# Kernel tuning notes

Measured on AMD Instinct MI355X. Metric: run time of the kernel, lower is better.

The kernel has to match this reference:

```python
import jax, jax.numpy as jnp
import numpy as np

NBIN = 256
EPS = 1e-10


def _diffhist(img, hmin, hmax):
    # Soft (linear-interpolation) histogram, faithful to torch index_add version.
    img = img.ravel()
    keep = (img >= hmin) & (img <= hmax)
    dh = (hmax - hmin) / (NBIN - 1)
    x = (img - hmin) / dh
    idx = jnp.floor(x)
    d = x - idx  # fractional part, carries the gradient
    # zero-weight + clamped index instead of boolean compaction (jit-friendly)
    idx_i = jnp.where(keep, idx.astype(jnp.int32), 0)
    w0 = jnp.where(keep, 1.0 - d, 0.0)
    w1 = jnp.where(keep, d, 0.0)
    h = jnp.zeros(NBIN + 1, dtype=img.dtype)
    h = h.at[idx_i].add(w0).at[idx_i + 1].add(w1)
    return h[:NBIN]


def setup_inputs() -> dict:
    key = jax.random.key(0)
    k0, k1 = jax.random.split(key)
    shape = (4, 256, 256, 256)
    img0 = jax.random.normal(k0, shape, dtype=jnp.float32)
    img1 = jax.random.normal(k1, shape, dtype=jnp.float32)
    return {"img0": img0, "img1": img1}


def reference(img0, img1):
    min0 = jnp.min(img0)  # differentiable, like torch.min
    h0 = _diffhist(img0, min0, 0.0)
    h1 = _diffhist(img1, min0, 0.0)
    h0 = (h0 + EPS) / (h0.sum() + EPS)
    h1 = (h1 + EPS) / (h1.sum() + EPS)
    # KLDivLoss(log_target=True, reduction='mean'):
    #   mean( exp(target) * (target - input) )
    inp = jnp.log((h1 + EPS) / h1)
    tgt = jnp.log((h1 + EPS) / h0)
    return jnp.mean(jnp.exp(tgt) * (tgt - inp))
```

## Files before the change

kernel.cpp:

```cpp
#include <hip/hip_runtime.h>

#define NBIN 256
#define EPSF 1e-10f
#define DSCALE 4096.0f
#define DSCALE_INV (1.0 / 4096.0)
#define DMASK ((1ull << 40) - 1)

__device__ __forceinline__ unsigned enc_f32(float f) {
    unsigned u = __float_as_uint(f);
    return (u & 0x80000000u) ? ~u : (u ^ 0x80000000u);
}
__device__ __forceinline__ float dec_f32(unsigned e) {
    unsigned u = (e & 0x80000000u) ? (e ^ 0x80000000u) : ~e;
    return __uint_as_float(u);
}

__global__ void init_kernel(unsigned* ws_min, unsigned long long* gh) {
    if (threadIdx.x == 0) *ws_min = 0xFFFFFFFFu;
    for (int j = threadIdx.x; j < 2 * NBIN; j += blockDim.x) gh[j] = 0ull;
}

__global__ void __launch_bounds__(256) min_kernel(const float4* __restrict__ img0,
                                                  long n4, unsigned* ws_min) {
    long stride = (long)gridDim.x * blockDim.x;
    long i = (long)blockIdx.x * blockDim.x + threadIdx.x;
    float m = __int_as_float(0x7f800000);
    if (i < n4) {
        float4 cur = img0[i];
        long j = i + stride;
        for (; j < n4; j += stride) {
            float4 nxt = img0[j];
            m = fminf(m, fminf(fminf(cur.x, cur.y), fminf(cur.z, cur.w)));
            cur = nxt;
        }
        m = fminf(m, fminf(fminf(cur.x, cur.y), fminf(cur.z, cur.w)));
    }
    for (int off = 32; off; off >>= 1) m = fminf(m, __shfl_xor(m, off));
    __shared__ float sm[4];
    int lane = threadIdx.x & 63, wid = threadIdx.x >> 6;
    if (lane == 0) sm[wid] = m;
    __syncthreads();
    if (threadIdx.x == 0) {
        float bm = fminf(fminf(sm[0], sm[1]), fminf(sm[2], sm[3]));
        atomicMin(ws_min, enc_f32(bm));
    }
}

__device__ __forceinline__ void hadd(float v, float hmin, float inv_dh,
                                     unsigned* h) {
    if (v >= hmin && v <= 0.f) {
        float x = (v - hmin) * inv_dh;
        float fi = floorf(x);
        int idx = (int)fi;
        unsigned di = __float2uint_rn((x - fi) * DSCALE);
        atomicAdd(&h[idx], (1u << 24) | di);
    }
}

__global__ void __launch_bounds__(256) hist_kernel(const float4* __restrict__ img0,
                                                   const float4* __restrict__ img1,
                                                   long n4, const unsigned* ws_min,
                                                   unsigned long long* __restrict__ gh) {
    __shared__ unsigned lh[4][2][NBIN];
    int tid = threadIdx.x;
    int wid = tid >> 6;
    unsigned* base = &lh[0][0][0];
    for (int j = tid; j < 4 * 2 * NBIN; j += 256) base[j] = 0u;
    __syncthreads();

    float hmin = dec_f32(*ws_min);
    float dh = (0.f - hmin) / (NBIN - 1);
    float inv_dh = 1.0f / dh;

    long stride = (long)gridDim.x * blockDim.x;
    unsigned* h0 = &lh[wid][0][0];
    unsigned* h1 = &lh[wid][1][0];

    long i = (long)blockIdx.x * blockDim.x + tid;
    if (i < n4) {
        float4 a = img0[i];
        float4 b = img1[i];
        long j = i + stride;
        for (; j < n4; j += stride) {
            float4 an = img0[j];
            float4 bn = img1[j];
            hadd(a.x, hmin, inv_dh, h0);
            hadd(a.y, hmin, inv_dh, h0);
            hadd(a.z, hmin, inv_dh, h0);
            hadd(a.w, hmin, inv_dh, h0);
            hadd(b.x, hmin, inv_dh, h1);
            hadd(b.y, hmin, inv_dh, h1);
            hadd(b.z, hmin, inv_dh, h1);
            hadd(b.w, hmin, inv_dh, h1);
            a = an;
            b = bn;
        }
        hadd(a.x, hmin, inv_dh, h0);
        hadd(a.y, hmin, inv_dh, h0);
        hadd(a.z, hmin, inv_dh, h0);
        hadd(a.w, hmin, inv_dh, h0);
        hadd(b.x, hmin, inv_dh, h1);
        hadd(b.y, hmin, inv_dh, h1);
        hadd(b.z, hmin, inv_dh, h1);
        hadd(b.w, hmin, inv_dh, h1);
    }
    __syncthreads();

    for (int b = tid; b < NBIN; b += 256) {
        unsigned long long c0 = 0, f0 = 0, c1 = 0, f1 = 0;
        for (int w = 0; w < 4; ++w) {
            unsigned p0 = lh[w][0][b];
            unsigned p1 = lh[w][1][b];
            c0 += p0 >> 24; f0 += p0 & 0xFFFFFFu;
            c1 += p1 >> 24; f1 += p1 & 0xFFFFFFu;
        }
        atomicAdd(&gh[b], (c0 << 40) | f0);
        atomicAdd(&gh[NBIN + b], (c1 << 40) | f1);
    }
}

__global__ void __launch_bounds__(256) kl_kernel(const unsigned long long* __restrict__ gh,
                                                 float* __restrict__ out) {
    int i = threadIdx.x;
    unsigned long long p0 = gh[i];
    unsigned long long p1 = gh[NBIN + i];
    unsigned long long q0 = (i > 0) ? gh[i - 1] : 0ull;
    unsigned long long q1 = (i > 0) ? gh[NBIN + i - 1] : 0ull;
    float h0 = (float)((double)(p0 >> 40) - (double)(p0 & DMASK) * DSCALE_INV
                       + (double)(q0 & DMASK) * DSCALE_INV);
    float h1 = (float)((double)(p1 >> 40) - (double)(p1 & DMASK) * DSCALE_INV
                       + (double)(q1 & DMASK) * DSCALE_INV);

    __shared__ float sw[4];
    int lane = i & 63, wid = i >> 6;

    float v = h0;
    for (int off = 32; off; off >>= 1) v += __shfl_xor(v, off);
    if (lane == 0) sw[wid] = v;
    __syncthreads();
    float s0 = sw[0] + sw[1] + sw[2] + sw[3];
    __syncthreads();

    v = h1;
    for (int off = 32; off; off >>= 1) v += __shfl_xor(v, off);
    if (lane == 0) sw[wid] = v;
    __syncthreads();
    float s1 = sw[0] + sw[1] + sw[2] + sw[3];
    __syncthreads();

    float a = (h0 + EPSF) / (s0 + EPSF);
    float b = (h1 + EPSF) / (s1 + EPSF);
    float tgt = logf((b + EPSF) / a);
    float inp = logf((b + EPSF) / b);
    float term = expf(tgt) * (tgt - inp);

    v = term;
    for (int off = 32; off; off >>= 1) v += __shfl_xor(v, off);
    if (lane == 0) sw[wid] = v;
    __syncthreads();
    if (i == 0) out[0] = (sw[0] + sw[1] + sw[2] + sw[3]) / (float)NBIN;
}

extern "C" void kernel_launch(void* const* d_in, const int* in_sizes, int n_in,
                              void* d_out, int out_size, void* d_ws, size_t ws_size,
                              hipStream_t stream) {
    const float* img0 = (const float*)d_in[0];
    const float* img1 = (const float*)d_in[1];
    float* out = (float*)d_out;
    unsigned* ws_min = (unsigned*)d_ws;
    unsigned long long* gh = (unsigned long long*)((char*)d_ws + 16);

    long n = (long)in_sizes[0];
    long n4 = n / 4;

    init_kernel<<<1, 256, 0, stream>>>(ws_min, gh);
    min_kernel<<<2048, 256, 0, stream>>>((const float4*)img0, n4, ws_min);
    hist_kernel<<<2048, 256, 0, stream>>>((const float4*)img0, (const float4*)img1,
                                          n4, ws_min, gh);
    kl_kernel<<<1, 256, 0, stream>>>(gh, out);
}
```

Before: 197.7 us.

## Replace shared atomics with per-quad private histograms and DPP lane merging

The histogram kernel now gives each group of 4 lanes its own private shared-memory histogram column (64 columns per image). Duplicate bins inside a quad are merged with DPP lane swizzles, so only one lane per distinct bin does a plain read-modify-write instead of an LDS atomic. The grid shrinks to 256 blocks, loads are prefetched two iterations ahead, and the packed count field moves to a 22-bit fractional layout. In exchange it uses 128KB of shared memory per block, which limits occupancy, adds a 64-way reduction at the end, and relies on the quad lanes within a column never racing.

```diff
diff --git a/kernel.cpp b/kernel.cpp
--- a/kernel.cpp
+++ b/kernel.cpp
@@ -1,6 +1,7 @@
 #include <hip/hip_runtime.h>
 
 #define NBIN 256
+#define NCOL 64
 #define EPSF 1e-10f
 #define DSCALE 4096.0f
 #define DSCALE_INV (1.0 / 4096.0)
@@ -16,8 +17,9 @@
 }
 
 __global__ void init_kernel(unsigned* ws_min, unsigned long long* gh) {
-    if (threadIdx.x == 0) *ws_min = 0xFFFFFFFFu;
-    for (int j = threadIdx.x; j < 2 * NBIN; j += blockDim.x) gh[j] = 0ull;
+    if (threadIdx.x == 0 && blockIdx.x == 0) *ws_min = 0xFFFFFFFFu;
+    int t = blockIdx.x * blockDim.x + threadIdx.x;
+    for (int j = t; j < 2 * NBIN; j += gridDim.x * blockDim.x) gh[j] = 0ull;
 }
 
 __global__ void __launch_bounds__(256) min_kernel(const float4* __restrict__ img0,
@@ -46,76 +48,82 @@
     }
 }
 
-__device__ __forceinline__ void hadd(float v, float hmin, float inv_dh,
-                                     unsigned* h) {
-    if (v >= hmin && v <= 0.f) {
-        float x = (v - hmin) * inv_dh;
-        float fi = floorf(x);
-        int idx = (int)fi;
-        unsigned di = __float2uint_rn((x - fi) * DSCALE);
-        atomicAdd(&h[idx], (1u << 24) | di);
-    }
+__device__ __forceinline__ void hrmw(float v, float hmin, float inv_dh,
+                                     unsigned* tab, int lpos) {
+    bool keep = (v >= hmin) && (v <= 0.f);
+    float x = (v - hmin) * inv_dh;
+    x = fminf(fmaxf(x, 0.f), 255.f);
+    float fi = floorf(x);
+    int idx = (int)fi;
+    unsigned di = __float2uint_rn((x - fi) * DSCALE);
+    unsigned pv = keep ? ((1u << 22) | di) : 0u;
+
+    int i1 = __builtin_amdgcn_update_dpp(0, idx, 0xB1, 0xF, 0xF, true);
+    int p1 = __builtin_amdgcn_update_dpp(0, (int)pv, 0xB1, 0xF, 0xF, true);
+    int i2 = __builtin_amdgcn_update_dpp(0, idx, 0x4E, 0xF, 0xF, true);
+    int p2 = __builtin_amdgcn_update_dpp(0, (int)pv, 0x4E, 0xF, 0xF, true);
+    int i3 = __builtin_amdgcn_update_dpp(0, idx, 0x1B, 0xF, 0xF, true);
+    int p3 = __builtin_amdgcn_update_dpp(0, (int)pv, 0x1B, 0xF, 0xF, true);
+    bool eq1 = (idx == i1), eq2 = (idx == i2), eq3 = (idx == i3);
+    unsigned tot = pv + (eq1 ? (unsigned)p1 : 0u)
+                      + (eq2 ? (unsigned)p2 : 0u)
+                      + (eq3 ? (unsigned)p3 : 0u);
+    bool notldr = (eq1 && (lpos & 1)) || ((eq2 || eq3) && (lpos & 2));
+    if (!notldr) tab[idx] += tot;
 }
 
 __global__ void __launch_bounds__(256) hist_kernel(const float4* __restrict__ img0,
                                                    const float4* __restrict__ img1,
                                                    long n4, const unsigned* ws_min,
                                                    unsigned long long* __restrict__ gh) {
-    __shared__ unsigned lh[4][2][NBIN];
+    __shared__ unsigned lh[2][NCOL][NBIN];
     int tid = threadIdx.x;
-    int wid = tid >> 6;
+    int col = tid >> 2;
+    int lpos = tid & 3;
     unsigned* base = &lh[0][0][0];
-    for (int j = tid; j < 4 * 2 * NBIN; j += 256) base[j] = 0u;
+    for (int j = tid; j < 2 * NCOL * NBIN; j += 256) base[j] = 0u;
     __syncthreads();
 
     float hmin = dec_f32(*ws_min);
     float dh = (0.f - hmin) / (NBIN - 1);
     float inv_dh = 1.0f / dh;
 
+    unsigned* t0 = &lh[0][col][0];
+    unsigned* t1 = &lh[1][col][0];
+
     long stride = (long)gridDim.x * blockDim.x;
-    unsigned* h0 = &lh[wid][0][0];
-    unsigned* h1 = &lh[wid][1][0];
+    long i = (long)blockIdx.x * blockDim.x + tid;
 
-    long i = (long)blockIdx.x * blockDim.x + tid;
-    if (i < n4) {
-        float4 a = img0[i];
-        float4 b = img1[i];
-        long j = i + stride;
-        for (; j < n4; j += stride) {
-            float4 an = img0[j];
-            float4 bn = img1[j];
-            hadd(a.x, hmin, inv_dh, h0);
-            hadd(a.y, hmin, inv_dh, h0);
-            hadd(a.z, hmin, inv_dh, h0);
-            hadd(a.w, hmin, inv_dh, h0);
-            hadd(b.x, hmin, inv_dh, h1);
-            hadd(b.y, hmin, inv_dh, h1);
-            hadd(b.z, hmin, inv_dh, h1);
-            hadd(b.w, hmin, inv_dh, h1);
-            a = an;
-            b = bn;
-        }
-        hadd(a.x, hmin, inv_dh, h0);
-        hadd(a.y, hmin, inv_dh, h0);
-        hadd(a.z, hmin, inv_dh, h0);
-        hadd(a.w, hmin, inv_dh, h0);
-        hadd(b.x, hmin, inv_dh, h1);
-        hadd(b.y, hmin, inv_dh, h1);
-        hadd(b.z, hmin, inv_dh, h1);
-        hadd(b.w, hmin, inv_dh, h1);
+    float4 ac, bc, an, bn;
+    if (i < n4) { ac = img0[i]; bc = img1[i]; }
+    if (i + stride < n4) { an = img0[i + stride]; bn = img1[i + stride]; }
+    for (; i < n4; i += stride) {
+        long ipp = i + 2 * stride;
+        float4 ap, bp;
+        bool has = ipp < n4;
+        if (has) { ap = img0[ipp]; bp = img1[ipp]; }
+        hrmw(ac.x, hmin, inv_dh, t0, lpos);
+        hrmw(ac.y, hmin, inv_dh, t0, lpos);
+        hrmw(ac.z, hmin, inv_dh, t0, lpos);
+        hrmw(ac.w, hmin, inv_dh, t0, lpos);
+        hrmw(bc.x, hmin, inv_dh, t1, lpos);
+        hrmw(bc.y, hmin, inv_dh, t1, lpos);
+        hrmw(bc.z, hmin, inv_dh, t1, lpos);
+        hrmw(bc.w, hmin, inv_dh, t1, lpos);
+        ac = an; bc = bn;
+        an = ap; bn = bp;
     }
     __syncthreads();
 
-    for (int b = tid; b < NBIN; b += 256) {
-        unsigned long long c0 = 0, f0 = 0, c1 = 0, f1 = 0;
-        for (int w = 0; w < 4; ++w) {
-            unsigned p0 = lh[w][0][b];
-            unsigned p1 = lh[w][1][b];
-            c0 += p0 >> 24; f0 += p0 & 0xFFFFFFu;
-            c1 += p1 >> 24; f1 += p1 & 0xFFFFFFu;
+    for (int p = tid; p < 2 * NBIN; p += 256) {
+        int im = p >> 8, b = p & 255;
+        unsigned long long c = 0, f = 0;
+        for (int cidx = 0; cidx < NCOL; ++cidx) {
+            unsigned u = lh[im][cidx][b];
+            c += u >> 22;
+            f += u & 0x3FFFFFu;
         }
-        atomicAdd(&gh[b], (c0 << 40) | f0);
-        atomicAdd(&gh[NBIN + b], (c1 << 40) | f1);
+        atomicAdd(&gh[im * NBIN + b], (c << 40) | f);
     }
 }
 
@@ -173,9 +181,9 @@
     long n = (long)in_sizes[0];
     long n4 = n / 4;
 
-    init_kernel<<<1, 256, 0, stream>>>(ws_min, gh);
+    init_kernel<<<4, 256, 0, stream>>>(ws_min, gh);
     min_kernel<<<2048, 256, 0, stream>>>((const float4*)img0, n4, ws_min);
-    hist_kernel<<<2048, 256, 0, stream>>>((const float4*)img0, (const float4*)img1,
-                                          n4, ws_min, gh);
+    hist_kernel<<<256, 256, 0, stream>>>((const float4*)img0, (const float4*)img1,
+                                         n4, ws_min, gh);
     kl_kernel<<<1, 256, 0, stream>>>(gh, out);
 }
```

Measured after the change: 431.6 us. 2.18x slower.
